# Kernel tuning notes

Measured on AMD Instinct MI355X. Metric: run time of the kernel, lower is better.

## Reference

```python
import jax, jax.numpy as jnp
import numpy as np
import math

B, T, C = 2, 2048, 1024
H = 16
D = C // H

def setup_inputs() -> dict:
    key = jax.random.key(0)
    k1, k2, k3, k4, k5 = jax.random.split(key, 5)
    scale = 0.02
    return {
        "x": jax.random.normal(k1, (B, T, C), dtype=jnp.float32),
        "w_attn": jax.random.normal(k2, (3 * C, C), dtype=jnp.float32) * scale,
        "b_attn": jax.random.normal(k3, (3 * C,), dtype=jnp.float32) * scale,
        "w_proj": jax.random.normal(k4, (C, C), dtype=jnp.float32) * scale,
        "b_proj": jax.random.normal(k5, (C,), dtype=jnp.float32) * scale,
    }

def reference(x, w_attn, b_attn, w_proj, b_proj):
    b, t, c = x.shape
    # c_attn: torch Linear -> x @ W.T + b, output [b, t, 3c]
    qkv = jnp.einsum('btc,fc->btf', x, w_attn) + b_attn
    # einops 'b t (a h d) -> a b h t d' with a=3, h=H
    qkv = qkv.reshape(b, t, 3, H, D).transpose(2, 0, 3, 1, 4)
    q, k, v = qkv[0], qkv[1], qkv[2]  # each [b, h, t, d]
    att = jnp.einsum('bhtd,bhsd->bhts', q, k) * (1.0 / math.sqrt(D))
    # causal mask: positions s > t are masked
    mask = jnp.tril(jnp.ones((t, t), dtype=bool))
    att = jnp.where(mask[None, None, :, :], att, jnp.float32(-jnp.inf))
    att = jax.nn.softmax(att, axis=-1)
    y = jnp.einsum('bhts,bhsd->bhtd', att, v)  # [b, h, t, d]
    y = y.transpose(0, 2, 1, 3).reshape(b, t, c)
    return jnp.einsum('btc,fc->btf', y, w_proj) + b_proj
```

## Files before the change

### kernel.cpp

```cpp
#include <hip/hip_runtime.h>
#include <stdint.h>

typedef unsigned short u16;
typedef __attribute__((ext_vector_type(8))) __bf16 bvec8;
typedef __attribute__((ext_vector_type(4))) float f32x4;

__device__ __forceinline__ u16 f32_to_bf16(float f) {
    uint32_t u = __float_as_uint(f);
    u += 0x7fffu + ((u >> 16) & 1u);
    return (u16)(u >> 16);
}

__device__ __forceinline__ void gl2lds16(const u16* g, u16* l) {
    void* gnc = const_cast<void*>((const void*)g);
    __builtin_amdgcn_global_load_lds(
        (__attribute__((address_space(1))) uint32_t*)gnc,
        (__attribute__((address_space(3))) uint32_t*)((void*)l),
        16, 0, 0);
}

__global__ __launch_bounds__(256) void cvt3(
    const float* __restrict__ a, int na4, const float* __restrict__ b, int nb4,
    const float* __restrict__ c, int nc4,
    u16* __restrict__ oa, u16* __restrict__ ob, u16* __restrict__ oc)
{
    int i = blockIdx.x * 256 + threadIdx.x;
    const float* src; u16* dst; int off;
    if (i < na4)             { src = a; dst = oa; off = i; }
    else if (i < na4 + nb4)  { src = b; dst = ob; off = i - na4; }
    else if (i < na4 + nb4 + nc4) { src = c; dst = oc; off = i - na4 - nb4; }
    else return;
    float4 v = ((const float4*)src)[off];
    ushort4 o;
    o.x = f32_to_bf16(v.x); o.y = f32_to_bf16(v.y);
    o.z = f32_to_bf16(v.z); o.w = f32_to_bf16(v.w);
    ((ushort4*)dst)[off] = o;
}

template <int BNt, bool OUT_BF16>
__global__ __launch_bounds__(256) void gemm_bt_bias(
    const u16* __restrict__ A, const u16* __restrict__ B,
    const float* __restrict__ bias, void* __restrict__ Cv,
    int M, int N, int K)
{
    constexpr int NT = BNt / 32;
    __shared__ __attribute__((aligned(16))) u16 As[128 * 32];
    __shared__ __attribute__((aligned(16))) u16 Bs[BNt * 32];

    const int tid = threadIdx.x, wave = tid >> 6, lane = tid & 63;
    const int col = lane & 15, quad = lane >> 4;
    const int m0 = blockIdx.y * 128, n0 = blockIdx.x * BNt;
    const int wm = (wave >> 1) * 64, wn = (wave & 1) * (BNt / 2);
    const int srow = lane >> 2, schunk = lane & 3;
    const u16* Ag = A + (size_t)(m0 + wave * 32) * K;

    f32x4 acc[4][NT];
#pragma unroll
    for (int i = 0; i < 4; i++)
#pragma unroll
        for (int j = 0; j < NT; j++) acc[i][j] = f32x4{0.f, 0.f, 0.f, 0.f};

    for (int k0 = 0; k0 < K; k0 += 32) {
        __syncthreads();
        gl2lds16(Ag + (size_t)(srow)      * K + k0 + schunk * 8, &As[(wave * 2 + 0) * 512]);
        gl2lds16(Ag + (size_t)(16 + srow) * K + k0 + schunk * 8, &As[(wave * 2 + 1) * 512]);
        if constexpr (BNt == 128) {
            const u16* Bg = B + (size_t)(n0 + wave * 32) * K;
            gl2lds16(Bg + (size_t)(srow)      * K + k0 + schunk * 8, &Bs[(wave * 2 + 0) * 512]);
            gl2lds16(Bg + (size_t)(16 + srow) * K + k0 + schunk * 8, &Bs[(wave * 2 + 1) * 512]);
        } else {
            const u16* Bg = B + (size_t)(n0 + wave * 16) * K;
            gl2lds16(Bg + (size_t)(srow)      * K + k0 + schunk * 8, &Bs[wave * 512]);
        }
        __syncthreads();

        bvec8 af[4], bfv[NT];
#pragma unroll
        for (int mt = 0; mt < 4; mt++)  af[mt]  = *(const bvec8*)&As[(wm + mt * 16 + col) * 32 + quad * 8];
#pragma unroll
        for (int nt = 0; nt < NT; nt++) bfv[nt] = *(const bvec8*)&Bs[(wn + nt * 16 + col) * 32 + quad * 8];
#pragma unroll
        for (int mt = 0; mt < 4; mt++)
#pragma unroll
            for (int nt = 0; nt < NT; nt++)
                acc[mt][nt] = __builtin_amdgcn_mfma_f32_16x16x32_bf16(af[mt], bfv[nt], acc[mt][nt], 0, 0, 0);
    }

#pragma unroll
    for (int mt = 0; mt < 4; mt++) {
#pragma unroll
        for (int r = 0; r < 4; r++) {
            const int m = m0 + wm + mt * 16 + quad * 4 + r;
#pragma unroll
            for (int nt = 0; nt < NT; nt++) {
                const int n = n0 + wn + nt * 16 + col;
                float v = acc[mt][nt][r] + bias[n];
                if (OUT_BF16) ((u16*)Cv)[(size_t)m * N + n] = f32_to_bf16(v);
                else          ((float*)Cv)[(size_t)m * N + n] = v;
            }
        }
    }
}

__global__ __launch_bounds__(256) void transpose_v(const u16* __restrict__ qkv,
                                                   u16* __restrict__ vT)
{
    __shared__ u16 Ts[64 * 74];
    const int tid = threadIdx.x;
    const int t0 = blockIdx.x * 64, h = blockIdx.y, b = blockIdx.z;
    const u16* src = qkv + (size_t)b * 2048 * 3072 + 2048 + h * 64;
#pragma unroll
    for (int k2 = 0; k2 < 2; k2++) {
        int c = k2 * 256 + tid, tl = c >> 3, ch = c & 7;
        *(uint4*)&Ts[tl * 74 + ch * 8] = *(const uint4*)(src + (size_t)(t0 + tl) * 3072 + ch * 8);
    }
    __syncthreads();
    u16* dst = vT + (size_t)((b * 16 + h) * 64) * 2048;
#pragma unroll
    for (int k2 = 0; k2 < 2; k2++) {
        int c = k2 * 256 + tid, d = c >> 3, tch = c & 7;
        u16 tmp[8];
#pragma unroll
        for (int j2 = 0; j2 < 8; j2++) tmp[j2] = Ts[(tch * 8 + j2) * 74 + d];
        *(uint4*)&dst[(size_t)d * 2048 + t0 + tch * 8] = *(const uint4*)tmp;
    }
}

__global__ __launch_bounds__(256) void attn_kernel(const u16* __restrict__ qkv,
                                                   const u16* __restrict__ vT,
                                                   u16* __restrict__ Y)
{
    __shared__ __attribute__((aligned(16))) u16 Qs[64 * 64];
    __shared__ __attribute__((aligned(16))) u16 Ks[2][64 * 64];
    __shared__ __attribute__((aligned(16))) u16 Vs[2][64 * 64];

    const int tid = threadIdx.x, wave = tid >> 6, lane = tid & 63;
    const int col = lane & 15, quad = lane >> 4;

    const int g = blockIdx.x;
    const int b = g >> 4, h = g & 15;
    const int s_idx = blockIdx.y;

    const u16* qb = qkv + (size_t)b * 2048 * 3072;
    const u16* vb = vT + (size_t)g * 64 * 2048;

    const int c0 = wave * 64 + lane, c1 = 256 + c0;
    const int r0 = c0 >> 3, p0 = c0 & 7, r1 = c1 >> 3, p1 = c1 & 7;
    const int sw0 = (p0 ^ (r0 & 7)) * 8, sw1 = (p1 ^ (r1 & 7)) * 8;
    const int tau0 = (r0 & 32) | ((r0 & 12) << 1) | ((r0 & 16) >> 2) | (r0 & 3);
    const int tau1 = (r1 & 32) | ((r1 & 12) << 1) | ((r1 & 16) >> 2) | (r1 & 3);

    const int q8 = quad * 8;
    const int qit = wave * 16 + col;

#pragma unroll
    for (int phase = 0; phase < 2; ++phase) {
        const int qt = phase ? (31 - s_idx) : s_idx;
        const int q0 = qt * 64;

        __syncthreads();
        gl2lds16(qb + (size_t)(q0 + r0) * 3072 + h * 64 + sw0, &Qs[wave * 512]);
        gl2lds16(qb + (size_t)(q0 + r1) * 3072 + h * 64 + sw1, &Qs[2048 + wave * 512]);
        __syncthreads();

        const int qrow = wave * 16 + col;
        bvec8 qf0 = *(const bvec8*)&Qs[qrow * 64 + ((quad       ^ (qrow & 7)) * 8)];
        bvec8 qf1 = *(const bvec8*)&Qs[qrow * 64 + (((4 + quad) ^ (qrow & 7)) * 8)];

        float l_acc = 0.f;
        f32x4 o[4];
#pragma unroll
        for (int d = 0; d < 4; d++) o[d] = f32x4{0.f, 0.f, 0.f, 0.f};

        {
            gl2lds16(qb + (size_t)(tau0) * 3072 + 1024 + h * 64 + sw0, &Ks[0][wave * 512]);
            gl2lds16(qb + (size_t)(tau1) * 3072 + 1024 + h * 64 + sw1, &Ks[0][2048 + wave * 512]);
            gl2lds16(vb + (size_t)r0 * 2048 + sw0, &Vs[0][wave * 512]);
            gl2lds16(vb + (size_t)r1 * 2048 + sw1, &Vs[0][2048 + wave * 512]);
        }

        for (int kt = 0; kt <= qt; ++kt) {
            const int cur = kt & 1;
            if (kt < qt) {
                const int s0n = (kt + 1) * 64;
                const int nb2 = cur ^ 1;
                gl2lds16(qb + (size_t)(s0n + tau0) * 3072 + 1024 + h * 64 + sw0, &Ks[nb2][wave * 512]);
                gl2lds16(qb + (size_t)(s0n + tau1) * 3072 + 1024 + h * 64 + sw1, &Ks[nb2][2048 + wave * 512]);
                gl2lds16(vb + (size_t)r0 * 2048 + s0n + sw0, &Vs[nb2][wave * 512]);
                gl2lds16(vb + (size_t)r1 * 2048 + s0n + sw1, &Vs[nb2][2048 + wave * 512]);
                asm volatile("s_waitcnt vmcnt(4)" ::: "memory");
            } else {
                asm volatile("s_waitcnt vmcnt(0)" ::: "memory");
            }
            asm volatile("s_barrier" ::: "memory");

            f32x4 sv[4];
#pragma unroll
            for (int nt = 0; nt < 4; nt++) {
                const int krow = nt * 16 + col;
                bvec8 kf0 = *(const bvec8*)&Ks[cur][krow * 64 + ((quad       ^ (krow & 7)) * 8)];
                bvec8 kf1 = *(const bvec8*)&Ks[cur][krow * 64 + (((4 + quad) ^ (krow & 7)) * 8)];
                sv[nt] = f32x4{0.f, 0.f, 0.f, 0.f};
                sv[nt] = __builtin_amdgcn_mfma_f32_16x16x32_bf16(kf0, qf0, sv[nt], 0, 0, 0);
                sv[nt] = __builtin_amdgcn_mfma_f32_16x16x32_bf16(kf1, qf1, sv[nt], 0, 0, 0);
            }

            const bool diag = (kt == qt);
            bvec8 pbv[2];
#pragma unroll
            for (int nt = 0; nt < 4; nt++) {
#pragma unroll
                for (int r = 0; r < 4; r++) {
                    float p = __expf(sv[nt][r] * 0.125f);
                    const int klog = 32 * (nt >> 1) + q8 + 4 * (nt & 1) + r;
                    if (diag && klog > qit) p = 0.f;
                    l_acc += p;
                    pbv[nt >> 1][(nt & 1) * 4 + r] = (__bf16)p;
                }
            }

#pragma unroll
            for (int ks = 0; ks < 2; ks++) {
#pragma unroll
                for (int d = 0; d < 4; d++) {
                    const int vrow = d * 16 + col;
                    bvec8 vf = *(const bvec8*)&Vs[cur][vrow * 64 + (((ks * 4 + quad) ^ (vrow & 7)) * 8)];
                    o[d] = __builtin_amdgcn_mfma_f32_16x16x32_bf16(pbv[ks], vf, o[d], 0, 0, 0);
                }
            }
            asm volatile("s_barrier" ::: "memory");
        }

        float l = l_acc;
        l += __shfl_xor(l, 16);
        l += __shfl_xor(l, 32);
#pragma unroll
        for (int r = 0; r < 4; r++) {
            const float lr = __shfl(l, quad * 4 + r);
            const float inv = 1.0f / lr;
            const int t = q0 + wave * 16 + quad * 4 + r;
#pragma unroll
            for (int d = 0; d < 4; d++)
                Y[(size_t)(b * 2048 + t) * 1024 + h * 64 + d * 16 + col] =
                    f32_to_bf16(o[d][r] * inv);
        }
    }
}

extern "C" void kernel_launch(void* const* d_in, const int* in_sizes, int n_in,
                              void* d_out, int out_size, void* d_ws, size_t ws_size,
                              hipStream_t stream) {
    const float* x      = (const float*)d_in[0];
    const float* w_attn = (const float*)d_in[1];
    const float* b_attn = (const float*)d_in[2];
    const float* w_proj = (const float*)d_in[3];
    const float* b_proj = (const float*)d_in[4];
    float* out = (float*)d_out;

    u16* xb  = (u16*)d_ws;
    u16* wab = xb  + (size_t)4096 * 1024;
    u16* wpb = wab + (size_t)3072 * 1024;
    u16* qkv = wpb + (size_t)1024 * 1024;
    u16* y   = qkv + (size_t)4096 * 3072;
    u16* vT  = xb;

    const int na4 = 4096 * 1024 / 4, nb4 = 3072 * 1024 / 4, nc4 = 1024 * 1024 / 4;
    cvt3<<<(na4 + nb4 + nc4 + 255) / 256, 256, 0, stream>>>(
        x, na4, w_attn, nb4, w_proj, nc4, xb, wab, wpb);

    dim3 g1(3072 / 128, 4096 / 128);
    gemm_bt_bias<128, true><<<g1, 256, 0, stream>>>(xb, wab, b_attn, qkv, 4096, 3072, 1024);

    dim3 gt(32, 16, 2);
    transpose_v<<<gt, 256, 0, stream>>>(qkv, vT);

    dim3 g2(32, 16, 1);
    attn_kernel<<<g2, 256, 0, stream>>>(qkv, vT, y);

    dim3 g3(1024 / 64, 4096 / 128);
    gemm_bt_bias<64, false><<<g3, 256, 0, stream>>>(y, wpb, b_proj, out, 4096, 1024, 1024);
}
```

Measured before the change: 182.4 us.

## Double-buffer LDS tiles in GEMM to overlap global loads with MFMA

The bias GEMM now keeps two LDS buffers and prefetches the next K-slice with global_load_lds while the current slice feeds the MFMAs. Partial vmcnt waits and raw s_barrier replace the two __syncthreads per iteration. The goal is to hide global-to-LDS latency behind compute, at the cost of twice the shared memory, which may lower occupancy. The hand-counted vmcnt values and the missing LDS-read waits before the second barrier make correctness depend on what the compiler emits.

```diff
diff --git a/kernel.cpp b/kernel.cpp
--- a/kernel.cpp
+++ b/kernel.cpp
@@ -44,8 +44,8 @@
     int M, int N, int K)
 {
     constexpr int NT = BNt / 32;
-    __shared__ __attribute__((aligned(16))) u16 As[128 * 32];
-    __shared__ __attribute__((aligned(16))) u16 Bs[BNt * 32];
+    __shared__ __attribute__((aligned(16))) u16 As[2][128 * 32];
+    __shared__ __attribute__((aligned(16))) u16 Bs[2][BNt * 32];
 
     const int tid = threadIdx.x, wave = tid >> 6, lane = tid & 63;
     const int col = lane & 15, quad = lane >> 4;
@@ -53,6 +53,7 @@
     const int wm = (wave >> 1) * 64, wn = (wave & 1) * (BNt / 2);
     const int srow = lane >> 2, schunk = lane & 3;
     const u16* Ag = A + (size_t)(m0 + wave * 32) * K;
+    const u16* Bg = B + (size_t)(n0 + wave * (BNt == 128 ? 32 : 16)) * K;
 
     f32x4 acc[4][NT];
 #pragma unroll
@@ -60,30 +61,43 @@
 #pragma unroll
         for (int j = 0; j < NT; j++) acc[i][j] = f32x4{0.f, 0.f, 0.f, 0.f};
 
-    for (int k0 = 0; k0 < K; k0 += 32) {
-        __syncthreads();
-        gl2lds16(Ag + (size_t)(srow)      * K + k0 + schunk * 8, &As[(wave * 2 + 0) * 512]);
-        gl2lds16(Ag + (size_t)(16 + srow) * K + k0 + schunk * 8, &As[(wave * 2 + 1) * 512]);
+    auto stage = [&](int bb, int k0) {
+        gl2lds16(Ag + (size_t)(srow)      * K + k0 + schunk * 8, &As[bb][(wave * 2 + 0) * 512]);
+        gl2lds16(Ag + (size_t)(16 + srow) * K + k0 + schunk * 8, &As[bb][(wave * 2 + 1) * 512]);
         if constexpr (BNt == 128) {
-            const u16* Bg = B + (size_t)(n0 + wave * 32) * K;
-            gl2lds16(Bg + (size_t)(srow)      * K + k0 + schunk * 8, &Bs[(wave * 2 + 0) * 512]);
-            gl2lds16(Bg + (size_t)(16 + srow) * K + k0 + schunk * 8, &Bs[(wave * 2 + 1) * 512]);
+            gl2lds16(Bg + (size_t)(srow)      * K + k0 + schunk * 8, &Bs[bb][(wave * 2 + 0) * 512]);
+            gl2lds16(Bg + (size_t)(16 + srow) * K + k0 + schunk * 8, &Bs[bb][(wave * 2 + 1) * 512]);
         } else {
-            const u16* Bg = B + (size_t)(n0 + wave * 16) * K;
-            gl2lds16(Bg + (size_t)(srow)      * K + k0 + schunk * 8, &Bs[wave * 512]);
-        }
-        __syncthreads();
+            gl2lds16(Bg + (size_t)(srow)      * K + k0 + schunk * 8, &Bs[bb][wave * 512]);
+        }
+    };
+
+    stage(0, 0);
+    const int NS = K / 32;
+
+    for (int t = 0; t < NS; ++t) {
+        const int cur = t & 1;
+        if (t + 1 < NS) {
+            stage(cur ^ 1, (t + 1) * 32);
+            if constexpr (BNt == 128) asm volatile("s_waitcnt vmcnt(4)" ::: "memory");
+            else                      asm volatile("s_waitcnt vmcnt(3)" ::: "memory");
+        } else {
+            asm volatile("s_waitcnt vmcnt(0)" ::: "memory");
+        }
+        asm volatile("s_barrier" ::: "memory");
 
         bvec8 af[4], bfv[NT];
 #pragma unroll
-        for (int mt = 0; mt < 4; mt++)  af[mt]  = *(const bvec8*)&As[(wm + mt * 16 + col) * 32 + quad * 8];
-#pragma unroll
-        for (int nt = 0; nt < NT; nt++) bfv[nt] = *(const bvec8*)&Bs[(wn + nt * 16 + col) * 32 + quad * 8];
+        for (int mt = 0; mt < 4; mt++)  af[mt]  = *(const bvec8*)&As[cur][(wm + mt * 16 + col) * 32 + quad * 8];
+#pragma unroll
+        for (int nt = 0; nt < NT; nt++) bfv[nt] = *(const bvec8*)&Bs[cur][(wn + nt * 16 + col) * 32 + quad * 8];
 #pragma unroll
         for (int mt = 0; mt < 4; mt++)
 #pragma unroll
             for (int nt = 0; nt < NT; nt++)
                 acc[mt][nt] = __builtin_amdgcn_mfma_f32_16x16x32_bf16(af[mt], bfv[nt], acc[mt][nt], 0, 0, 0);
+
+        asm volatile("s_barrier" ::: "memory");
     }
 
 #pragma unroll
```

Result: no change. 181.5 us (-0.5%).
